# Kernel tuning notes

Measured on AMD Instinct MI355X. Metric: run time of the kernel, lower is better.

Reference implementation:

```python
import jax, jax.numpy as jnp
import numpy as np

B, S, D_IN, D_OUT, H = 4, 2048, 1024, 1024, 16
HD = D_OUT // H  # head_dim = 64


def setup_inputs() -> dict:
    key = jax.random.key(0)
    ks = jax.random.split(key, 6)
    scale = 1.0 / np.sqrt(D_IN)
    return {
        "x": jax.random.normal(ks[0], (B, S, D_IN), dtype=jnp.float32),
        "Wq": jax.random.normal(ks[1], (D_IN, D_OUT), dtype=jnp.float32) * scale,
        "Wk": jax.random.normal(ks[2], (D_IN, D_OUT), dtype=jnp.float32) * scale,
        "Wv": jax.random.normal(ks[3], (D_IN, D_OUT), dtype=jnp.float32) * scale,
        "Wo": jax.random.normal(ks[4], (D_OUT, D_OUT), dtype=jnp.float32) * (1.0 / np.sqrt(D_OUT)),
        "bo": jax.random.normal(ks[5], (D_OUT,), dtype=jnp.float32) * 0.02,
    }


def reference(x, Wq, Wk, Wv, Wo, bo):
    b, n, _ = x.shape
    h, hd = H, HD
    # projections -> (b, h, n, hd)
    q = (x @ Wq).reshape(b, n, h, hd).transpose(0, 2, 1, 3)
    k = (x @ Wk).reshape(b, n, h, hd).transpose(0, 2, 1, 3)
    v = (x @ Wv).reshape(b, n, h, hd).transpose(0, 2, 1, 3)
    # scores (b, h, n, n) with causal mask then scale (matches original order)
    scores = jnp.einsum("bhqd,bhkd->bhqk", q, k)
    causal = jnp.tril(jnp.ones((n, n), dtype=bool))  # True = keep
    scores = jnp.where(causal, scores, -jnp.inf) / jnp.sqrt(jnp.asarray(hd, x.dtype))
    attn = jax.nn.softmax(scores, axis=-1)
    ctx = jnp.einsum("bhqk,bhkd->bhqd", attn, v)
    ctx = ctx.transpose(0, 2, 1, 3).reshape(b, n, h * hd)
    return ctx @ Wo + bo
```

## Files before the change

### kernel.cpp

```cpp
#include <hip/hip_runtime.h>
#include <hip/hip_bf16.h>
#include <math.h>

typedef __attribute__((ext_vector_type(4))) float f32x4;
typedef __attribute__((ext_vector_type(16))) float f32x16;
typedef __attribute__((ext_vector_type(8))) short bf16x8;
typedef __attribute__((ext_vector_type(4))) unsigned int u32x4;

#define DEV __device__ __forceinline__
#define MFMA16 __builtin_amdgcn_mfma_f32_16x16x32_bf16
#define MFMA32 __builtin_amdgcn_mfma_f32_32x32x16_bf16
#define SBAR __builtin_amdgcn_s_barrier()
#define SCHED0 __builtin_amdgcn_sched_barrier(0)

constexpr int S      = 2048;
constexpr int DMODEL = 1024;
constexpr int HD     = 64;
constexpr int MROWS  = 4 * 2048;

DEV unsigned short f2bf(float f) {
  union { float f; unsigned int u; } v; v.f = f;
  unsigned int u = v.u;
  unsigned int r = u + 0x7fffu + ((u >> 16) & 1u);
  return (unsigned short)(r >> 16);
}

DEV unsigned int pkbf(float lo, float hi) {
  unsigned int r;
  asm("v_cvt_pk_bf16_f32 %0, %1, %2" : "=v"(r) : "v"(lo), "v"(hi));
  return r;
}

DEV float fexp2(float x) { return __builtin_amdgcn_exp2f(x); }

DEV void gload_lds16(const void* g, void* l) {
  __builtin_amdgcn_global_load_lds(
      (const __attribute__((address_space(1))) unsigned int*)g,
      (__attribute__((address_space(3))) unsigned int*)l, 16, 0, 0);
}

__global__ __launch_bounds__(256) void k_conv(const float* __restrict__ in,
                                              unsigned short* __restrict__ out) {
  int i = blockIdx.x * 256 + threadIdx.x;
  float4 v = ((const float4*)in)[i];
  ushort4 o;
  o.x = f2bf(v.x); o.y = f2bf(v.y); o.z = f2bf(v.z); o.w = f2bf(v.w);
  ((ushort4*)out)[i] = o;
}

__global__ __launch_bounds__(256) void k_transpose4(const float* __restrict__ Wq,
                                                    const float* __restrict__ Wk,
                                                    const float* __restrict__ Wv,
                                                    const float* __restrict__ Wo,
                                                    unsigned short* __restrict__ wt,
                                                    unsigned short* __restrict__ wot) {
  __shared__ float tile[32][33];
  const int z = blockIdx.z;
  const float* W = (z == 0) ? Wq : (z == 1) ? Wk : (z == 2) ? Wv : Wo;
  unsigned short* Wt = (z == 3) ? wot : wt + (size_t)z * DMODEL * DMODEL;
  int n0 = blockIdx.x * 32, k0 = blockIdx.y * 32;
  int tx = threadIdx.x, ty = threadIdx.y;
#pragma unroll
  for (int j = 0; j < 4; ++j)
    tile[ty + j * 8][tx] = W[(size_t)(k0 + ty + j * 8) * DMODEL + n0 + tx];
  __syncthreads();
#pragma unroll
  for (int j = 0; j < 4; ++j)
    Wt[(size_t)(n0 + ty + j * 8) * DMODEL + k0 + tx] = f2bf(tile[tx][ty + j * 8]);
}

template<int NBX, int EPI>
__global__ __launch_bounds__(512, 2) void k_gemm8(const unsigned short* __restrict__ A,
                                                  const unsigned short* __restrict__ Bt,
                                                  unsigned short* __restrict__ Qg,
                                                  unsigned short* __restrict__ Kg,
                                                  unsigned short* __restrict__ Vt,
                                                  const float* __restrict__ bo,
                                                  float* __restrict__ out) {
  __shared__ __align__(16) char lds[147456];
  const int tid = threadIdx.x, lane = tid & 63;
  const int wid = tid >> 6, wm = wid >> 1, wn = wid & 1;
  const int lq = lane & 15, lg = lane >> 4;
  const int flat = blockIdx.x;
  const int wg = (flat & 7) * (NBX * 4) + (flat >> 3);
  const int by = wg / NBX, bx = wg % NBX;
  const int m0 = by * 256, n0 = bx * 128;

  auto stageFull = [&](int kt, int buf) {
    char* dA = lds + buf * 49152;
    char* dB = dA + 32768;
    const unsigned short* gA = A + (size_t)m0 * DMODEL + kt * 64;
    const unsigned short* gB = Bt + (size_t)n0 * DMODEL + kt * 64;
#pragma unroll
    for (int i = 0; i < 4; ++i) {
      int c = tid + i * 512; int r = c >> 3, cc = c & 7;
      gload_lds16(gA + (size_t)r * DMODEL + ((cc ^ (r & 7)) << 3), dA + c * 16);
    }
#pragma unroll
    for (int i = 0; i < 2; ++i) {
      int c = tid + i * 512; int r = c >> 3, cc = c & 7;
      gload_lds16(gB + (size_t)r * DMODEL + ((cc ^ (r & 7)) << 3), dB + c * 16);
    }
  };
  auto stageHalf = [&](int kt, int buf, int half) {
    char* dA = lds + buf * 49152;
    char* dB = dA + 32768;
    const unsigned short* gA = A + (size_t)m0 * DMODEL + kt * 64;
    const unsigned short* gB = Bt + (size_t)n0 * DMODEL + kt * 64;
#pragma unroll
    for (int i = 0; i < 2; ++i) {
      int c = tid + (2 * half + i) * 512; int r = c >> 3, cc = c & 7;
      gload_lds16(gA + (size_t)r * DMODEL + ((cc ^ (r & 7)) << 3), dA + c * 16);
    }
    {
      int c = tid + half * 512; int r = c >> 3, cc = c & 7;
      gload_lds16(gB + (size_t)r * DMODEL + ((cc ^ (r & 7)) << 3), dB + c * 16);
    }
  };

  stageFull(0, 0);
  stageFull(1, 1);
  SCHED0;
  asm volatile("s_waitcnt vmcnt(6)" ::: "memory");
  SCHED0;
  SBAR;
  SCHED0;

  f32x4 acc[4][4] = {};
  int bcur = 0, bth = 2;
#pragma unroll 1
  for (int t = 0; t < 16; ++t) {
    const char* pA = lds + bcur * 49152;
    const char* pB = pA + 32768;
    {
      bf16x8 af[4], bfr[4];
#pragma unroll
      for (int mi = 0; mi < 4; ++mi) {
        int row = wm * 64 + mi * 16 + lq;
        af[mi] = *(const bf16x8*)(pA + row * 128 + ((lg ^ (row & 7)) << 4));
      }
#pragma unroll
      for (int ni = 0; ni < 4; ++ni) {
        int row = wn * 64 + ni * 16 + lq;
        bfr[ni] = *(const bf16x8*)(pB + row * 128 + ((lg ^ (row & 7)) << 4));
      }
      if (t < 14) stageHalf(t + 2, bth, 0);
      SBAR;
      asm volatile("s_waitcnt lgkmcnt(0)" ::: "memory");
      SCHED0;
      __builtin_amdgcn_s_setprio(1);
#pragma unroll
      for (int mi = 0; mi < 4; ++mi)
#pragma unroll
        for (int ni = 0; ni < 4; ++ni)
          acc[mi][ni] = MFMA16(af[mi], bfr[ni], acc[mi][ni], 0, 0, 0);
      __builtin_amdgcn_s_setprio(0);
      SCHED0;
    }
    {
      bf16x8 af[4], bfr[4];
#pragma unroll
      for (int mi = 0; mi < 4; ++mi) {
        int row = wm * 64 + mi * 16 + lq;
        af[mi] = *(const bf16x8*)(pA + row * 128 + (((4 + lg) ^ (row & 7)) << 4));
      }
#pragma unroll
      for (int ni = 0; ni < 4; ++ni) {
        int row = wn * 64 + ni * 16 + lq;
        bfr[ni] = *(const bf16x8*)(pB + row * 128 + (((4 + lg) ^ (row & 7)) << 4));
      }
      if (t < 14) stageHalf(t + 2, bth, 1);
      SBAR;
      asm volatile("s_waitcnt lgkmcnt(0)" ::: "memory");
      SCHED0;
      __builtin_amdgcn_s_setprio(1);
#pragma unroll
      for (int mi = 0; mi < 4; ++mi)
#pragma unroll
        for (int ni = 0; ni < 4; ++ni)
          acc[mi][ni] = MFMA16(af[mi], bfr[ni], acc[mi][ni], 0, 0, 0);
      __builtin_amdgcn_s_setprio(0);
      SCHED0;
    }
    if (t < 14) {
      asm volatile("s_waitcnt vmcnt(6)" ::: "memory");
    } else if (t == 14) {
      asm volatile("s_waitcnt vmcnt(0)" ::: "memory");
    }
    SCHED0;
    if (t < 15) SBAR;
    SCHED0;
    int nb = (bcur + 1 == 3) ? 0 : bcur + 1;
    int nt = (bth + 1 == 3) ? 0 : bth + 1;
    bcur = nb; bth = nt;
  }

  if (EPI == 0) {
#pragma unroll
    for (int mi = 0; mi < 4; ++mi)
#pragma unroll
      for (int ni = 0; ni < 4; ++ni) {
        int n = n0 + wn * 64 + ni * 16 + lq;
        int widx = n >> 10, nn = n & 1023;
        int h = nn >> 6, d = nn & 63;
        int mbase = m0 + wm * 64 + mi * 16 + lg * 4;
        int b_ = mbase >> 11, s_ = mbase & 2047;
        if (widx == 2) {
          ushort4 o;
          o.x = f2bf(acc[mi][ni][0]);
          o.y = f2bf(acc[mi][ni][1]);
          o.z = f2bf(acc[mi][ni][2]);
          o.w = f2bf(acc[mi][ni][3]);
          *(ushort4*)(Vt + ((size_t)((b_ * 16 + h) * 64 + d)) * S + s_) = o;
        } else {
          unsigned short* dst = (widx == 0) ? Qg : Kg;
          float scale = (widx == 0) ? 0.18033688f : 1.0f;
#pragma unroll
          for (int r = 0; r < 4; ++r)
            dst[(size_t)((b_ * 16 + h) * 2048 + s_ + r) * HD + d] = f2bf(acc[mi][ni][r] * scale);
        }
      }
  } else {
#pragma unroll
    for (int mi = 0; mi < 4; ++mi)
#pragma unroll
      for (int ni = 0; ni < 4; ++ni) {
        int n = n0 + wn * 64 + ni * 16 + lq;
        float bv = bo[n];
#pragma unroll
        for (int r = 0; r < 4; ++r) {
          int m = m0 + wm * 64 + mi * 16 + lg * 4 + r;
          out[(size_t)m * DMODEL + n] = acc[mi][ni][r] + bv;
        }
      }
  }
}

__global__ __launch_bounds__(512, 2) void k_attn(const unsigned short* __restrict__ Qg,
                                                 const unsigned short* __restrict__ Kg,
                                                 const unsigned short* __restrict__ Vt,
                                                 unsigned short* __restrict__ Ctx) {
  __shared__ __align__(16) char lds[32768];
  const int f = blockIdx.x;
  const int i4 = f & 255, hi2 = f >> 8;
  const int bh = i4 >> 2, q = i4 & 3;
  const int Qb = hi2 ? (7 - q) : q;
  const int tid = threadIdx.x;
  const int lane = tid & 63, w = tid >> 6;
  const int lq5 = lane & 31, hi = lane >> 5;
  const size_t base = (size_t)bh * (S * HD);
  const int b = bh >> 4, h = bh & 15;
  const int krow = tid >> 3, kcc = tid & 7, scc = kcc ^ (krow & 7);
  const int vd = tid >> 3;
  const int vfd = (vd & 7) ^ ((vd >> 3) & 7);
  const int vscc = (tid & 7) ^ vfd;
  const unsigned short* VtRow = Vt + (size_t)(bh * 64 + vd) * S;

  const int q0w = Qb * 256 + w * 32;
  const int tmax = 4 * Qb + 3;
  const int diag = q0w >> 6;

  bf16x8 qF[4];
#pragma unroll
  for (int dc = 0; dc < 4; ++dc)
    qF[dc] = *(const bf16x8*)(Qg + base + (size_t)(q0w + lq5) * HD + dc * 16 + hi * 8);

  f32x16 o0 = {}, o1 = {};
  float m_run = -INFINITY, l_run = 0.f;

  gload_lds16(Kg + base + (size_t)krow * HD + scc * 8, lds + tid * 16);
  gload_lds16(VtRow + vscc * 8, lds + 16384 + tid * 16);
  __syncthreads();

#pragma unroll 1
  for (int t = 0; t <= tmax; ++t) {
    const int cur = t & 1, nxt = cur ^ 1;
    char* sK  = lds + cur * 8192;
    char* sVT = lds + 16384 + cur * 8192;
    const bool have_next = (t < tmax);
    if (have_next) {
      gload_lds16(Kg + base + (size_t)((t + 1) * 64 + krow) * HD + scc * 8,
                  lds + nxt * 8192 + tid * 16);
      gload_lds16(VtRow + (t + 1) * 64 + vscc * 8,
                  lds + 16384 + nxt * 8192 + tid * 16);
    }
    const bool active = (t <= diag);
    if (active) {
      const bool isdiag = (t == diag);
      const int nkb = (isdiag && !(q0w & 32)) ? 1 : 2;
      f32x16 st0 = {}, st1 = {};
#pragma unroll
      for (int dc = 0; dc < 4; ++dc) {
        int row = lq5;
        bf16x8 a0 = *(const bf16x8*)(sK + row * 128 + (((2 * dc + hi) ^ (row & 7)) << 4));
        st0 = MFMA32(a0, qF[dc], st0, 0, 0, 0);
      }
      if (nkb == 2) {
#pragma unroll
        for (int dc = 0; dc < 4; ++dc) {
          int row = 32 + lq5;
          bf16x8 a1 = *(const bf16x8*)(sK + row * 128 + (((2 * dc + hi) ^ (row & 7)) << 4));
          st1 = MFMA32(a1, qF[dc], st1, 0, 0, 0);
        }
      }
      if (isdiag) {
        int qo = q0w + lq5 - t * 64;
        if (q0w & 32) {
#pragma unroll
          for (int r = 0; r < 16; ++r) {
            int key = 32 + (r & 3) + 8 * (r >> 2) + 4 * hi;
            st1[r] = (key > qo) ? -INFINITY : st1[r];
          }
        } else {
#pragma unroll
          for (int r = 0; r < 16; ++r) {
            int key = (r & 3) + 8 * (r >> 2) + 4 * hi;
            st0[r] = (key > qo) ? -INFINITY : st0[r];
          }
        }
      }
      float mx = st0[0];
#pragma unroll
      for (int r = 1; r < 16; ++r) mx = fmaxf(mx, st0[r]);
      if (nkb == 2) {
#pragma unroll
        for (int r = 0; r < 16; ++r) mx = fmaxf(mx, st1[r]);
      }
      mx = fmaxf(mx, __shfl_xor(mx, 32));
      bool need = !(mx <= m_run + 8.0f);
      if (__any(need)) {
        float mn = fmaxf(m_run, mx);
        float alpha = fexp2(m_run - mn);
        m_run = mn;
        l_run *= alpha;
#pragma unroll
        for (int r = 0; r < 16; ++r) { o0[r] *= alpha; o1[r] *= alpha; }
      }
      float rs[4] = {0.f, 0.f, 0.f, 0.f};
#pragma unroll
      for (int r = 0; r < 16; ++r) {
        float p = fexp2(st0[r] - m_run);
        st0[r] = p;
        rs[r & 3] += p;
      }
      if (nkb == 2) {
#pragma unroll
        for (int r = 0; r < 16; ++r) {
          float p = fexp2(st1[r] - m_run);
          st1[r] = p;
          rs[r & 3] += p;
        }
      }
      float rsum = (rs[0] + rs[1]) + (rs[2] + rs[3]);
      rsum += __shfl_xor(rsum, 32);
      l_run += rsum;
      {
        unsigned int wv[8];
#pragma unroll
        for (int j = 0; j < 8; ++j) wv[j] = pkbf(st0[2 * j], st0[2 * j + 1]);
        asm("v_permlane32_swap_b32 %0, %1" : "+v"(wv[0]), "+v"(wv[2]));
        asm("v_permlane32_swap_b32 %0, %1" : "+v"(wv[1]), "+v"(wv[3]));
        asm("v_permlane32_swap_b32 %0, %1" : "+v"(wv[4]), "+v"(wv[6]));
        asm("v_permlane32_swap_b32 %0, %1" : "+v"(wv[5]), "+v"(wv[7]));
        union { bf16x8 v; unsigned int u[4]; } fa, fb;
        fa.u[0] = wv[0]; fa.u[1] = wv[1]; fa.u[2] = wv[2]; fa.u[3] = wv[3];
        fb.u[0] = wv[4]; fb.u[1] = wv[5]; fb.u[2] = wv[6]; fb.u[3] = wv[7];
#pragma unroll
        for (int kc = 0; kc < 2; ++kc) {
          bf16x8 bp = kc ? fb.v : fa.v;
          {
            int d = lq5, fd = (d & 7) ^ ((d >> 3) & 7);
            bf16x8 av = *(const bf16x8*)(sVT + d * 128 + (((kc * 2 + hi) ^ fd) << 4));
            o0 = MFMA32(av, bp, o0, 0, 0, 0);
          }
          {
            int d = 32 + lq5, fd = (d & 7) ^ ((d >> 3) & 7);
            bf16x8 av = *(const bf16x8*)(sVT + d * 128 + (((kc * 2 + hi) ^ fd) << 4));
            o1 = MFMA32(av, bp, o1, 0, 0, 0);
          }
        }
      }
      if (nkb == 2) {
        unsigned int wv[8];
#pragma unroll
        for (int j = 0; j < 8; ++j) wv[j] = pkbf(st1[2 * j], st1[2 * j + 1]);
        asm("v_permlane32_swap_b32 %0, %1" : "+v"(wv[0]), "+v"(wv[2]));
        asm("v_permlane32_swap_b32 %0, %1" : "+v"(wv[1]), "+v"(wv[3]));
        asm("v_permlane32_swap_b32 %0, %1" : "+v"(wv[4]), "+v"(wv[6]));
        asm("v_permlane32_swap_b32 %0, %1" : "+v"(wv[5]), "+v"(wv[7]));
        union { bf16x8 v; unsigned int u[4]; } fa, fb;
        fa.u[0] = wv[0]; fa.u[1] = wv[1]; fa.u[2] = wv[2]; fa.u[3] = wv[3];
        fb.u[0] = wv[4]; fb.u[1] = wv[5]; fb.u[2] = wv[6]; fb.u[3] = wv[7];
#pragma unroll
        for (int kc = 0; kc < 2; ++kc) {
          bf16x8 bp = kc ? fb.v : fa.v;
          {
            int d = lq5, fd = (d & 7) ^ ((d >> 3) & 7);
            bf16x8 av = *(const bf16x8*)(sVT + d * 128 + ((((2 + kc) * 2 + hi) ^ fd) << 4));
            o0 = MFMA32(av, bp, o0, 0, 0, 0);
          }
          {
            int d = 32 + lq5, fd = (d & 7) ^ ((d >> 3) & 7);
            bf16x8 av = *(const bf16x8*)(sVT + d * 128 + ((((2 + kc) * 2 + hi) ^ fd) << 4));
            o1 = MFMA32(av, bp, o1, 0, 0, 0);
          }
        }
      }
    }
    __syncthreads();
  }

  __syncthreads();
  {
    float inv = 1.0f / l_run;
    char* slice = lds + w * 4096;
#pragma unroll
    for (int db = 0; db < 2; ++db)
#pragma unroll
      for (int j = 0; j < 8; ++j) {
        int d0 = (j & 1) * 2 + (j >> 1) * 8 + 4 * hi + 32 * db;
        float va = (db ? o1[2 * j] : o0[2 * j]) * inv;
        float vb = (db ? o1[2 * j + 1] : o0[2 * j + 1]) * inv;
        *(unsigned int*)(slice + lq5 * 128 + (((d0 >> 3) ^ (lq5 & 7)) << 4) + (d0 & 7) * 2) =
            pkbf(va, vb);
      }
    asm volatile("s_waitcnt lgkmcnt(0)" ::: "memory");
#pragma unroll
    for (int i = 0; i < 4; ++i) {
      int r = lane >> 1, cc = (lane & 1) * 4 + i;
      u32x4 v = *(const u32x4*)(slice + r * 128 + ((cc ^ (r & 7)) << 4));
      *(u32x4*)(Ctx + (size_t)(b * S + q0w + r) * DMODEL + h * HD + cc * 8) = v;
    }
  }
}

extern "C" void kernel_launch(void* const* d_in, const int* in_sizes, int n_in,
                              void* d_out, int out_size, void* d_ws, size_t ws_size,
                              hipStream_t stream) {
  const float* x  = (const float*)d_in[0];
  const float* Wq = (const float*)d_in[1];
  const float* Wk = (const float*)d_in[2];
  const float* Wv = (const float*)d_in[3];
  const float* Wo = (const float*)d_in[4];
  const float* bo = (const float*)d_in[5];
  float* out = (float*)d_out;

  char* p = (char*)d_ws;
  unsigned short* xb  = (unsigned short*)p; p += (size_t)MROWS * DMODEL * 2;
  unsigned short* wt  = (unsigned short*)p; p += (size_t)3 * DMODEL * DMODEL * 2;
  unsigned short* wot = (unsigned short*)p; p += (size_t)DMODEL * DMODEL * 2;
  unsigned short* qg  = (unsigned short*)p; p += (size_t)MROWS * DMODEL * 2;
  unsigned short* kg  = (unsigned short*)p; p += (size_t)MROWS * DMODEL * 2;
  unsigned short* vt  = (unsigned short*)p; p += (size_t)MROWS * DMODEL * 2;
  unsigned short* ctx = (unsigned short*)p; p += (size_t)MROWS * DMODEL * 2;

  k_conv<<<(MROWS * DMODEL) / 1024, 256, 0, stream>>>(x, xb);
  k_transpose4<<<dim3(32, 32, 4), dim3(32, 8), 0, stream>>>(Wq, Wk, Wv, Wo, wt, wot);
  k_gemm8<24, 0><<<768, 512, 0, stream>>>(xb, wt, qg, kg, vt, nullptr, nullptr);
  k_attn<<<512, 512, 0, stream>>>(qg, kg, vt, ctx);
  k_gemm8<8, 1><<<256, 512, 0, stream>>>(ctx, wot, nullptr, nullptr, nullptr, bo, out);
}
```

Baseline: 168.7 us.

## Triple-buffer K/V loads in attention and split GEMM template into two kernels

The attention kernel moves from double-buffered K/V staging with a full __syncthreads per iteration to a 3-stage ring. It prefetches two tiles ahead and uses explicit vmcnt waits plus a raw s_barrier, so global loads overlap more compute and less time is spent stalled at barriers. This raises LDS use from 32KB to 48KB per block, which could affect occupancy. The templated GEMM is split into separate QKV and output-projection kernels, with the output kernel getting its own simplified staging loop.

```diff
diff --git a/kernel.cpp b/kernel.cpp
--- a/kernel.cpp
+++ b/kernel.cpp
@@ -69,18 +69,16 @@
     Wt[(size_t)(n0 + ty + j * 8) * DMODEL + k0 + tx] = f2bf(tile[tx][ty + j * 8]);
 }
 
-template<int NBX, int EPI>
-__global__ __launch_bounds__(512, 2) void k_gemm8(const unsigned short* __restrict__ A,
-                                                  const unsigned short* __restrict__ Bt,
-                                                  unsigned short* __restrict__ Qg,
-                                                  unsigned short* __restrict__ Kg,
-                                                  unsigned short* __restrict__ Vt,
-                                                  const float* __restrict__ bo,
-                                                  float* __restrict__ out) {
+__global__ __launch_bounds__(512, 2) void k_gemmQKV(const unsigned short* __restrict__ A,
+                                                    const unsigned short* __restrict__ Bt,
+                                                    unsigned short* __restrict__ Qg,
+                                                    unsigned short* __restrict__ Kg,
+                                                    unsigned short* __restrict__ Vt) {
   __shared__ __align__(16) char lds[147456];
   const int tid = threadIdx.x, lane = tid & 63;
   const int wid = tid >> 6, wm = wid >> 1, wn = wid & 1;
   const int lq = lane & 15, lg = lane >> 4;
+  constexpr int NBX = 24;
   const int flat = blockIdx.x;
   const int wg = (flat & 7) * (NBX * 4) + (flat >> 3);
   const int by = wg / NBX, bx = wg % NBX;
@@ -195,52 +193,132 @@
     bcur = nb; bth = nt;
   }
 
-  if (EPI == 0) {
-#pragma unroll
-    for (int mi = 0; mi < 4; ++mi)
+#pragma unroll
+  for (int mi = 0; mi < 4; ++mi)
+#pragma unroll
+    for (int ni = 0; ni < 4; ++ni) {
+      int n = n0 + wn * 64 + ni * 16 + lq;
+      int widx = n >> 10, nn = n & 1023;
+      int h = nn >> 6, d = nn & 63;
+      int mbase = m0 + wm * 64 + mi * 16 + lg * 4;
+      int b_ = mbase >> 11, s_ = mbase & 2047;
+      if (widx == 2) {
+        ushort4 o;
+        o.x = f2bf(acc[mi][ni][0]);
+        o.y = f2bf(acc[mi][ni][1]);
+        o.z = f2bf(acc[mi][ni][2]);
+        o.w = f2bf(acc[mi][ni][3]);
+        *(ushort4*)(Vt + ((size_t)((b_ * 16 + h) * 64 + d)) * S + s_) = o;
+      } else {
+        unsigned short* dst = (widx == 0) ? Qg : Kg;
+        float scale = (widx == 0) ? 0.18033688f : 1.0f;
+#pragma unroll
+        for (int r = 0; r < 4; ++r)
+          dst[(size_t)((b_ * 16 + h) * 2048 + s_ + r) * HD + d] = f2bf(acc[mi][ni][r] * scale);
+      }
+    }
+}
+
+__global__ __launch_bounds__(512, 2) void k_gemmP(const unsigned short* __restrict__ A,
+                                                  const unsigned short* __restrict__ Bt,
+                                                  const float* __restrict__ bo,
+                                                  float* __restrict__ out) {
+  __shared__ __align__(16) char lds[147456];
+  const int tid = threadIdx.x, lane = tid & 63;
+  const int wid = tid >> 6, wm = wid >> 1, wn = wid & 1;
+  const int lq = lane & 15, lg = lane >> 4;
+  constexpr int NBX = 8;
+  const int flat = blockIdx.x;
+  const int wg = (flat & 7) * (NBX * 4) + (flat >> 3);
+  const int by = wg / NBX, bx = wg % NBX;
+  const int m0 = by * 256, n0 = bx * 128;
+
+  auto stage = [&](int kt, int buf) {
+    char* dA = lds + buf * 49152;
+    char* dB = dA + 32768;
+    const unsigned short* gA = A + (size_t)m0 * DMODEL + kt * 64;
+    const unsigned short* gB = Bt + (size_t)n0 * DMODEL + kt * 64;
+#pragma unroll
+    for (int i = 0; i < 4; ++i) {
+      int c = tid + i * 512; int r = c >> 3, cc = c & 7;
+      gload_lds16(gA + (size_t)r * DMODEL + ((cc ^ (r & 7)) << 3), dA + c * 16);
+    }
+#pragma unroll
+    for (int i = 0; i < 2; ++i) {
+      int c = tid + i * 512; int r = c >> 3, cc = c & 7;
+      gload_lds16(gB + (size_t)r * DMODEL + ((cc ^ (r & 7)) << 3), dB + c * 16);
+    }
+  };
+
+  stage(0, 0);
+  stage(1, 1);
+  SCHED0;
+  asm volatile("s_waitcnt vmcnt(6)" ::: "memory");
+  SCHED0;
+  SBAR;
+  SCHED0;
+
+  f32x4 acc[4][4] = {};
+  int bcur = 0, bth = 2;
+#pragma unroll 1
+  for (int t = 0; t < 16; ++t) {
+    if (t < 14) stage(t + 2, bth);
+    const char* pA = lds + bcur * 49152;
+    const char* pB = pA + 32768;
+#pragma unroll
+    for (int kk = 0; kk < 2; ++kk) {
+      bf16x8 af[4], bfr[4];
+#pragma unroll
+      for (int mi = 0; mi < 4; ++mi) {
+        int row = wm * 64 + mi * 16 + lq;
+        af[mi] = *(const bf16x8*)(pA + row * 128 + ((((kk << 2) + lg) ^ (row & 7)) << 4));
+      }
 #pragma unroll
       for (int ni = 0; ni < 4; ++ni) {
-        int n = n0 + wn * 64 + ni * 16 + lq;
-        int widx = n >> 10, nn = n & 1023;
-        int h = nn >> 6, d = nn & 63;
-        int mbase = m0 + wm * 64 + mi * 16 + lg * 4;
-        int b_ = mbase >> 11, s_ = mbase & 2047;
-        if (widx == 2) {
-          ushort4 o;
-          o.x = f2bf(acc[mi][ni][0]);
-          o.y = f2bf(acc[mi][ni][1]);
-          o.z = f2bf(acc[mi][ni][2]);
-          o.w = f2bf(acc[mi][ni][3]);
-          *(ushort4*)(Vt + ((size_t)((b_ * 16 + h) * 64 + d)) * S + s_) = o;
-        } else {
-          unsigned short* dst = (widx == 0) ? Qg : Kg;
-          float scale = (widx == 0) ? 0.18033688f : 1.0f;
-#pragma unroll
-          for (int r = 0; r < 4; ++r)
-            dst[(size_t)((b_ * 16 + h) * 2048 + s_ + r) * HD + d] = f2bf(acc[mi][ni][r] * scale);
-        }
-      }
-  } else {
-#pragma unroll
-    for (int mi = 0; mi < 4; ++mi)
-#pragma unroll
-      for (int ni = 0; ni < 4; ++ni) {
-        int n = n0 + wn * 64 + ni * 16 + lq;
-        float bv = bo[n];
-#pragma unroll
-        for (int r = 0; r < 4; ++r) {
-          int m = m0 + wm * 64 + mi * 16 + lg * 4 + r;
-          out[(size_t)m * DMODEL + n] = acc[mi][ni][r] + bv;
-        }
-      }
+        int row = wn * 64 + ni * 16 + lq;
+        bfr[ni] = *(const bf16x8*)(pB + row * 128 + ((((kk << 2) + lg) ^ (row & 7)) << 4));
+      }
+      __builtin_amdgcn_s_setprio(1);
+#pragma unroll
+      for (int mi = 0; mi < 4; ++mi)
+#pragma unroll
+        for (int ni = 0; ni < 4; ++ni)
+          acc[mi][ni] = MFMA16(af[mi], bfr[ni], acc[mi][ni], 0, 0, 0);
+      __builtin_amdgcn_s_setprio(0);
+    }
+    SCHED0;
+    if (t < 14) {
+      asm volatile("s_waitcnt vmcnt(6)" ::: "memory");
+    } else if (t == 14) {
+      asm volatile("s_waitcnt vmcnt(0)" ::: "memory");
+    }
+    SCHED0;
+    if (t < 15) SBAR;
+    SCHED0;
+    int nb = (bcur + 1 == 3) ? 0 : bcur + 1;
+    int nt = (bth + 1 == 3) ? 0 : bth + 1;
+    bcur = nb; bth = nt;
   }
+
+#pragma unroll
+  for (int mi = 0; mi < 4; ++mi)
+#pragma unroll
+    for (int ni = 0; ni < 4; ++ni) {
+      int n = n0 + wn * 64 + ni * 16 + lq;
+      float bv = bo[n];
+#pragma unroll
+      for (int r = 0; r < 4; ++r) {
+        int m = m0 + wm * 64 + mi * 16 + lg * 4 + r;
+        out[(size_t)m * DMODEL + n] = acc[mi][ni][r] + bv;
+      }
+    }
 }
 
 __global__ __launch_bounds__(512, 2) void k_attn(const unsigned short* __restrict__ Qg,
                                                  const unsigned short* __restrict__ Kg,
                                                  const unsigned short* __restrict__ Vt,
                                                  unsigned short* __restrict__ Ctx) {
-  __shared__ __align__(16) char lds[32768];
+  __shared__ __align__(16) char lds[49152];
   const int f = blockIdx.x;
   const int i4 = f & 255, hi2 = f >> 8;
   const int bh = i4 >> 2, q = i4 & 3;
@@ -260,6 +338,13 @@
   const int tmax = 4 * Qb + 3;
   const int diag = q0w >> 6;
 
+  auto stageKV = [&](int t, int buf) {
+    gload_lds16(Kg + base + (size_t)(t * 64 + krow) * HD + scc * 8,
+                lds + buf * 8192 + tid * 16);
+    gload_lds16(VtRow + t * 64 + vscc * 8,
+                lds + 24576 + buf * 8192 + tid * 16);
+  };
+
   bf16x8 qF[4];
 #pragma unroll
   for (int dc = 0; dc < 4; ++dc)
@@ -268,22 +353,21 @@
   f32x16 o0 = {}, o1 = {};
   float m_run = -INFINITY, l_run = 0.f;
 
-  gload_lds16(Kg + base + (size_t)krow * HD + scc * 8, lds + tid * 16);
-  gload_lds16(VtRow + vscc * 8, lds + 16384 + tid * 16);
-  __syncthreads();
+  stageKV(0, 0);
+  stageKV(1, 1);
+  SCHED0;
+  asm volatile("s_waitcnt vmcnt(2)" ::: "memory");
+  SCHED0;
+  SBAR;
+  SCHED0;
 
 #pragma unroll 1
   for (int t = 0; t <= tmax; ++t) {
-    const int cur = t & 1, nxt = cur ^ 1;
+    const int cur = t % 3;
     char* sK  = lds + cur * 8192;
-    char* sVT = lds + 16384 + cur * 8192;
-    const bool have_next = (t < tmax);
-    if (have_next) {
-      gload_lds16(Kg + base + (size_t)((t + 1) * 64 + krow) * HD + scc * 8,
-                  lds + nxt * 8192 + tid * 16);
-      gload_lds16(VtRow + (t + 1) * 64 + vscc * 8,
-                  lds + 16384 + nxt * 8192 + tid * 16);
-    }
+    char* sVT = lds + 24576 + cur * 8192;
+    const bool stg = (t + 2 <= tmax);
+    if (stg) stageKV(t + 2, (t + 2) % 3);
     const bool active = (t <= diag);
     if (active) {
       const bool isdiag = (t == diag);
@@ -407,7 +491,15 @@
         }
       }
     }
-    __syncthreads();
+    SCHED0;
+    if (stg) {
+      asm volatile("s_waitcnt vmcnt(2)" ::: "memory");
+    } else if (t + 1 <= tmax) {
+      asm volatile("s_waitcnt vmcnt(0)" ::: "memory");
+    }
+    SCHED0;
+    if (t < tmax) SBAR;
+    SCHED0;
   }
 
   __syncthreads();
@@ -456,7 +548,7 @@
 
   k_conv<<<(MROWS * DMODEL) / 1024, 256, 0, stream>>>(x, xb);
   k_transpose4<<<dim3(32, 32, 4), dim3(32, 8), 0, stream>>>(Wq, Wk, Wv, Wo, wt, wot);
-  k_gemm8<24, 0><<<768, 512, 0, stream>>>(xb, wt, qg, kg, vt, nullptr, nullptr);
+  k_gemmQKV<<<768, 512, 0, stream>>>(xb, wt, qg, kg, vt);
   k_attn<<<512, 512, 0, stream>>>(qg, kg, vt, ctx);
-  k_gemm8<8, 1><<<256, 512, 0, stream>>>(ctx, wot, nullptr, nullptr, nullptr, bo, out);
-}
+  k_gemmP<<<256, 512, 0, stream>>>(ctx, wot, bo, out);
+}
```

New measurement: 171.1 us. Within noise of the previous version (+1.4%).
